# Kernel optimization log

Hardware: AMD Instinct MI355X
Metric: run time of the kernel (lower is better)

Reference implementation:

```python
import jax, jax.numpy as jnp
import numpy as np

D_MODEL = 1024
NUM_HEADS = 16
LN_EPS = 1e-5


def setup_inputs() -> dict:
    key = jax.random.key(0)
    ks = jax.random.split(key, 7)
    B, S, D = 8, 1024, D_MODEL
    x = jax.random.normal(ks[0], (B, S, D), dtype=jnp.float32)
    # LayerNorm params (torch defaults: weight=1, bias=0; randomize slightly)
    ln_gamma = jnp.ones((D,), jnp.float32) + 0.02 * jax.random.normal(ks[1], (D,), jnp.float32)
    ln_beta = 0.02 * jax.random.normal(ks[2], (D,), jnp.float32)
    # nn.MultiheadAttention params: packed in_proj [3D, D], out_proj [D, D]
    scale = 1.0 / np.sqrt(D)
    in_proj_w = scale * jax.random.normal(ks[3], (3 * D, D), dtype=jnp.float32)
    in_proj_b = jnp.zeros((3 * D,), jnp.float32)
    out_proj_w = scale * jax.random.normal(ks[4], (D, D), dtype=jnp.float32)
    out_proj_b = jnp.zeros((D,), jnp.float32)
    return {
        "x": x,
        "ln_gamma": ln_gamma,
        "ln_beta": ln_beta,
        "in_proj_w": in_proj_w,
        "in_proj_b": in_proj_b,
        "out_proj_w": out_proj_w,
        "out_proj_b": out_proj_b,
    }


def reference(x, ln_gamma, ln_beta, in_proj_w, in_proj_b, out_proj_w, out_proj_b):
    B, S, D = x.shape
    H = NUM_HEADS
    Dh = D // H

    residual = x
    # LayerNorm (torch eps=1e-5)
    mu = jnp.mean(x, axis=-1, keepdims=True)
    var = jnp.mean(jnp.square(x - mu), axis=-1, keepdims=True)
    xn = (x - mu) * jax.lax.rsqrt(var + LN_EPS) * ln_gamma + ln_beta

    # Packed QKV projection: y = xn @ in_proj_w.T + in_proj_b
    qkv = jnp.einsum("bsd,ed->bse", xn, in_proj_w) + in_proj_b  # [B,S,3D]
    q, k, v = jnp.split(qkv, 3, axis=-1)

    def heads(t):  # [B,S,D] -> [B,H,S,Dh]
        return t.reshape(B, S, H, Dh).transpose(0, 2, 1, 3)

    q, k, v = heads(q), heads(k), heads(v)

    scores = jnp.einsum("bhsd,bhtd->bhst", q, k) / np.sqrt(Dh)  # [B,H,S,S]
    probs = jax.nn.softmax(scores, axis=-1)
    ctx = jnp.einsum("bhst,bhtd->bhsd", probs, v)  # [B,H,S,Dh]
    ctx = ctx.transpose(0, 2, 1, 3).reshape(B, S, D)

    attn_out = jnp.einsum("bsd,ed->bse", ctx, out_proj_w) + out_proj_b
    # (need_weights=True would also expose probs.mean over heads; math above
    #  matches the explicit non-flash path torch falls back to)
    return attn_out + residual
```

## Files before the change

kernel.cpp:

```cpp
#include <hip/hip_runtime.h>
#include <hip/hip_bf16.h>

typedef __bf16 bf16;
typedef __bf16 bf16x8 __attribute__((ext_vector_type(8)));
typedef __bf16 bf16x4 __attribute__((ext_vector_type(4)));
typedef float  f32x4  __attribute__((ext_vector_type(4)));

#define D_MODEL 1024
#define S_LEN   1024
#define NHEAD   16
#define DH      64

#define AS1 __attribute__((address_space(1)))
#define AS3 __attribute__((address_space(3)))

__global__ __launch_bounds__(256) void ln_cvt_kernel(
        const float* __restrict__ x, const float* __restrict__ gamma,
        const float* __restrict__ beta, bf16* __restrict__ xn,
        const float* __restrict__ w1, bf16* __restrict__ o1, int n1,
        const float* __restrict__ w2, bf16* __restrict__ o2, int n2) {
    const int tid = threadIdx.x;
    if (blockIdx.x < 8192) {
        const int row = blockIdx.x;
        const float4 v = ((const float4*)(x + (size_t)row * D_MODEL))[tid];
        float s  = v.x + v.y + v.z + v.w;
        float s2 = v.x*v.x + v.y*v.y + v.z*v.z + v.w*v.w;
        #pragma unroll
        for (int d = 1; d < 64; d <<= 1) { s += __shfl_xor(s, d); s2 += __shfl_xor(s2, d); }
        __shared__ float red[8];
        const int wave = tid >> 6;
        if ((tid & 63) == 0) { red[wave] = s; red[4 + wave] = s2; }
        __syncthreads();
        s  = red[0] + red[1] + red[2] + red[3];
        s2 = red[4] + red[5] + red[6] + red[7];
        const float mu   = s * (1.0f / D_MODEL);
        const float var  = s2 * (1.0f / D_MODEL) - mu * mu;
        const float rstd = rsqrtf(var + 1e-5f);
        const float4 g = ((const float4*)gamma)[tid];
        const float4 b = ((const float4*)beta)[tid];
        bf16x4 o;
        o[0] = (bf16)((v.x - mu) * rstd * g.x + b.x);
        o[1] = (bf16)((v.y - mu) * rstd * g.y + b.y);
        o[2] = (bf16)((v.z - mu) * rstd * g.z + b.z);
        o[3] = (bf16)((v.w - mu) * rstd * g.w + b.w);
        ((bf16x4*)(xn + (size_t)row * D_MODEL))[tid] = o;
    } else {
        int i = (blockIdx.x - 8192) * 256 + tid;
        const int stride = 1024 * 256;
        for (; i < n1 + n2; i += stride) {
            const float4 v = (i < n1) ? ((const float4*)w1)[i] : ((const float4*)w2)[i - n1];
            bf16x4 r;
            r[0] = (bf16)v.x; r[1] = (bf16)v.y; r[2] = (bf16)v.z; r[3] = (bf16)v.w;
            if (i < n1) ((bf16x4*)o1)[i] = r; else ((bf16x4*)o2)[i - n1] = r;
        }
    }
}

#define GEMM_MAIN_LOOP(Ab, Wb, K)                                                        \
    f32x4 acc[4][4] = {};                                                                \
    for (int kt = 0; kt < (K); kt += 64) {                                               \
        _Pragma("unroll")                                                                \
        for (int i = 0; i < 4; ++i) {                                                    \
            const int L = i * 256 + tid;                                                 \
            const int r = L >> 3, blk = L & 7;                                           \
            const int src = (blk ^ (r & 7)) * 8;                                         \
            __builtin_amdgcn_global_load_lds(                                            \
                (const AS1 void*)((Ab) + (size_t)r * (K) + kt + src),                    \
                (AS3 void*)(As + L * 8), 16, 0, 0);                                      \
            __builtin_amdgcn_global_load_lds(                                            \
                (const AS1 void*)((Wb) + (size_t)r * (K) + kt + src),                    \
                (AS3 void*)(Bs + L * 8), 16, 0, 0);                                      \
        }                                                                                \
        __syncthreads();                                                                 \
        _Pragma("unroll")                                                                \
        for (int kk = 0; kk < 2; ++kk) {                                                 \
            bf16x8 af[4], bfm[4];                                                        \
            _Pragma("unroll")                                                            \
            for (int m = 0; m < 4; ++m) {                                                \
                const int R = wr * 64 + m * 16 + (lane & 15);                            \
                af[m] = *(const bf16x8*)(As + R * 64 +                                   \
                            (((kk * 4 + (lane >> 4)) ^ (R & 7)) << 3));                  \
            }                                                                            \
            _Pragma("unroll")                                                            \
            for (int n = 0; n < 4; ++n) {                                                \
                const int R = wc * 64 + n * 16 + (lane & 15);                            \
                bfm[n] = *(const bf16x8*)(Bs + R * 64 +                                  \
                            (((kk * 4 + (lane >> 4)) ^ (R & 7)) << 3));                  \
            }                                                                            \
            _Pragma("unroll")                                                            \
            for (int m = 0; m < 4; ++m)                                                  \
                _Pragma("unroll")                                                        \
                for (int n = 0; n < 4; ++n)                                              \
                    acc[m][n] = __builtin_amdgcn_mfma_f32_16x16x32_bf16(                 \
                        af[m], bfm[n], acc[m][n], 0, 0, 0);                              \
        }                                                                                \
        __syncthreads();                                                                 \
    }

#define XCD_REMAP()                                                                      \
    const int f = blockIdx.y * gridDim.x + blockIdx.x;                                   \
    const int xcd = f & 7;                                                               \
    const int rank = f >> 3;                                                             \
    const int brow = (xcd * 8 + (rank & 7)) * 128;                                       \
    const int bcol = (rank >> 3) * 128;

__global__ __launch_bounds__(256, 4) void gemm_qkv(
        const bf16* __restrict__ A, const bf16* __restrict__ W,
        const float* __restrict__ bias,
        bf16* __restrict__ q, bf16* __restrict__ k, bf16* __restrict__ vt) {
    __shared__ bf16 smem[2 * 128 * 64];
    bf16* As = smem;
    bf16* Bs = smem + 128 * 64;
    const int tid = threadIdx.x;
    const int lane = tid & 63;
    const int wave = tid >> 6;
    const int wr = wave >> 1, wc = wave & 1;
    XCD_REMAP()
    const bf16* Ab = A + (size_t)brow * 1024;
    const bf16* Wb = W + (size_t)bcol * 1024;

    GEMM_MAIN_LOOP(Ab, Wb, 1024)

    const int region = bcol >> 10;
    const int c = lane & 15, hh = lane >> 4;
    if (region == 2) {
        #pragma unroll
        for (int m = 0; m < 4; ++m) {
            #pragma unroll
            for (int n = 0; n < 4; ++n) {
                const int col = bcol + wc * 64 + n * 16 + c;
                const float bb = bias[col];
                const int e = col & 1023;
                const int h = e >> 6, dh = e & 63;
                const int row0 = brow + wr * 64 + m * 16 + hh * 4;
                const int b = row0 >> 10, s0 = row0 & 1023;
                const int bh = b * NHEAD + h;
                bf16x4 pk;
                #pragma unroll
                for (int j = 0; j < 4; ++j) pk[j] = (bf16)(acc[m][n][j] + bb);
                *(bf16x4*)(vt + ((size_t)bh * DH + dh) * S_LEN + s0) = pk;
            }
        }
    } else {
        const float qsc = (region == 0) ? 0.1803368801111244f : 1.0f;
        #pragma unroll
        for (int m = 0; m < 4; ++m) {
            #pragma unroll
            for (int n = 0; n < 4; ++n) {
                const int col = wc * 64 + n * 16 + c;
                const float bb = bias[bcol + col];
                #pragma unroll
                for (int j = 0; j < 4; ++j) {
                    const int row = wr * 64 + m * 16 + hh * 4 + j;
                    const int pb = (col >> 3) ^ (row & 7);
                    smem[row * 128 + pb * 8 + (col & 7)] = (bf16)((acc[m][n][j] + bb) * qsc);
                }
            }
        }
        __syncthreads();
        bf16* dst = (region == 0) ? q : k;
        #pragma unroll
        for (int i = 0; i < 8; ++i) {
            const int idx = i * 256 + tid;
            const int row = idx >> 4;
            const int bb = idx & 15;
            const bf16x8 vv = *(const bf16x8*)(smem + row * 128 + (bb ^ (row & 7)) * 8);
            const int grow = brow + row;
            const int s = grow & 1023, b = grow >> 10;
            const int col0 = bcol + bb * 8;
            const int e = col0 & 1023;
            const int h = e >> 6, dh = e & 63;
            *(bf16x8*)(dst + ((size_t)(b * NHEAD + h) * S_LEN + s) * DH + dh) = vv;
        }
    }
}

__global__ __launch_bounds__(256, 4) void gemm_out(
        const bf16* __restrict__ A, const bf16* __restrict__ W,
        const float* __restrict__ bias, const float* __restrict__ resid,
        float* __restrict__ out) {
    __shared__ bf16 smem[2 * 128 * 64];
    bf16* As = smem;
    bf16* Bs = smem + 128 * 64;
    const int tid = threadIdx.x;
    const int lane = tid & 63;
    const int wave = tid >> 6;
    const int wr = wave >> 1, wc = wave & 1;
    XCD_REMAP()
    const bf16* Ab = A + (size_t)brow * 1024;
    const bf16* Wb = W + (size_t)bcol * 1024;

    GEMM_MAIN_LOOP(Ab, Wb, 1024)

    #pragma unroll
    for (int m = 0; m < 4; ++m) {
        #pragma unroll
        for (int n = 0; n < 4; ++n) {
            const int col = bcol + wc * 64 + n * 16 + (lane & 15);
            const float bb = bias[col];
            #pragma unroll
            for (int j = 0; j < 4; ++j) {
                const int row = brow + wr * 64 + m * 16 + (lane >> 4) * 4 + j;
                const size_t idx = (size_t)row * D_MODEL + col;
                out[idx] = acc[m][n][j] + bb + resid[idx];
            }
        }
    }
}

__global__ __launch_bounds__(512, 4) void attn_kernel(
        const bf16* __restrict__ Q, const bf16* __restrict__ Kv,
        const bf16* __restrict__ Vt, bf16* __restrict__ ctx) {
    __shared__ bf16 KsB[2][64 * 64];
    __shared__ bf16 VsB[2][64 * 64];
    __shared__ bf16 PtB[8][32 * 64];
    const int tid = threadIdx.x;
    const int lane = tid & 63;
    const int w = tid >> 6;
    const int c = lane & 15;
    const int h = lane >> 4;
    const int bh = blockIdx.x;
    const int bb = bh >> 4, hd = bh & 15;
    const int q0 = blockIdx.y * 256 + w * 32;

    const bf16* Qh = Q + ((size_t)bh * S_LEN + q0) * DH;
    const char* Kb = (const char*)(Kv + (size_t)bh * S_LEN * DH);
    const char* Vb = (const char*)(Vt + (size_t)bh * DH * S_LEN);
    char* pw = (char*)&PtB[w][0];

    bf16x8 qf[2][2];
    #pragma unroll
    for (int nq = 0; nq < 2; ++nq)
        #pragma unroll
        for (int kk = 0; kk < 2; ++kk)
            qf[nq][kk] = *(const bf16x8*)(Qh + (16 * nq + c) * DH + kk * 32 + h * 8);

    bf16x8 ones;
    #pragma unroll
    for (int j = 0; j < 8; ++j) ones[j] = (bf16)1.0f;

    f32x4 O[2][4] = {};
    f32x4 lacc[2] = {};

#define STAGE(BB, KT) do {                                                               \
    const int row = tid >> 3;                                                            \
    const int sw = ((tid & 7) ^ (row & 7)) << 4;                                         \
    __builtin_amdgcn_global_load_lds(                                                    \
        (const AS1 void*)(Kb + (size_t)((KT) + row) * 128 + sw),                         \
        (AS3 void*)((char*)&KsB[BB][0] + tid * 16), 16, 0, 0);                           \
    __builtin_amdgcn_global_load_lds(                                                    \
        (const AS1 void*)(Vb + (size_t)row * 2048 + (KT) * 2 + sw),                      \
        (AS3 void*)((char*)&VsB[BB][0] + tid * 16), 16, 0, 0);                           \
} while (0)

    STAGE(0, 0);
    for (int t = 0; t < 16; ++t) {
        if (t < 15) {
            STAGE((t + 1) & 1, (t + 1) * 64);
            asm volatile("s_waitcnt vmcnt(2)" ::: "memory");
        } else {
            asm volatile("s_waitcnt vmcnt(0)" ::: "memory");
        }
        __builtin_amdgcn_s_barrier();
        const char* Ksb = (const char*)&KsB[t & 1][0];
        const char* Vsb = (const char*)&VsB[t & 1][0];

        f32x4 sf[2][4] = {};
        __builtin_amdgcn_s_setprio(1);
        #pragma unroll
        for (int kk = 0; kk < 2; ++kk) {
            bf16x8 kf[4];
            #pragma unroll
            for (int a = 0; a < 4; ++a)
                kf[a] = *(const bf16x8*)(Ksb + (16 * a + c) * 128 +
                                         (((4 * kk + h) ^ (c & 7)) << 4));
            #pragma unroll
            for (int nq = 0; nq < 2; ++nq)
                #pragma unroll
                for (int a = 0; a < 4; ++a)
                    sf[nq][a] = __builtin_amdgcn_mfma_f32_16x16x32_bf16(
                        kf[a], qf[nq][kk], sf[nq][a], 0, 0, 0);
        }
        __builtin_amdgcn_s_setprio(0);

        #pragma unroll
        for (int nq = 0; nq < 2; ++nq) {
            #pragma unroll
            for (int a = 0; a < 4; ++a) {
                bf16x4 pk;
                #pragma unroll
                for (int r = 0; r < 4; ++r)
                    pk[r] = (bf16)__builtin_amdgcn_exp2f(sf[nq][a][r]);
                *(bf16x4*)(pw + (16 * nq + c) * 128 +
                           (((2 * a + (h >> 1)) ^ (c & 7)) << 4) + 8 * (h & 1)) = pk;
            }
        }

        __builtin_amdgcn_s_setprio(1);
        #pragma unroll
        for (int kk = 0; kk < 2; ++kk) {
            bf16x8 pf[2], vf[4];
            #pragma unroll
            for (int mq = 0; mq < 2; ++mq)
                pf[mq] = *(const bf16x8*)(pw + (16 * mq + c) * 128 +
                                          (((4 * kk + h) ^ (c & 7)) << 4));
            #pragma unroll
            for (int f2 = 0; f2 < 4; ++f2)
                vf[f2] = *(const bf16x8*)(Vsb + (16 * f2 + c) * 128 +
                                          (((4 * kk + h) ^ (c & 7)) << 4));
            #pragma unroll
            for (int mq = 0; mq < 2; ++mq) {
                #pragma unroll
                for (int f2 = 0; f2 < 4; ++f2)
                    O[mq][f2] = __builtin_amdgcn_mfma_f32_16x16x32_bf16(
                        pf[mq], vf[f2], O[mq][f2], 0, 0, 0);
                lacc[mq] = __builtin_amdgcn_mfma_f32_16x16x32_bf16(
                    pf[mq], ones, lacc[mq], 0, 0, 0);
            }
        }
        __builtin_amdgcn_s_setprio(0);
        asm volatile("s_waitcnt lgkmcnt(0)" ::: "memory");
        __builtin_amdgcn_s_barrier();
    }
#undef STAGE

    #pragma unroll
    for (int mq = 0; mq < 2; ++mq) {
        float iv[4];
        #pragma unroll
        for (int r = 0; r < 4; ++r) iv[r] = 1.0f / lacc[mq][r];
        #pragma unroll
        for (int f2 = 0; f2 < 4; ++f2)
            #pragma unroll
            for (int r = 0; r < 4; ++r) {
                const int s = q0 + 16 * mq + 4 * h + r;
                ctx[((size_t)(bb * S_LEN + s)) * D_MODEL + hd * DH + 16 * f2 + c] =
                    (bf16)(O[mq][f2][r] * iv[r]);
            }
    }
}

extern "C" void kernel_launch(void* const* d_in, const int* in_sizes, int n_in,
                              void* d_out, int out_size, void* d_ws, size_t ws_size,
                              hipStream_t stream) {
    const float* x     = (const float*)d_in[0];
    const float* gamma = (const float*)d_in[1];
    const float* beta  = (const float*)d_in[2];
    const float* in_w  = (const float*)d_in[3];
    const float* in_b  = (const float*)d_in[4];
    const float* out_w = (const float*)d_in[5];
    const float* out_b = (const float*)d_in[6];
    float* out = (float*)d_out;

    char* ws = (char*)d_ws;
    bf16* wq  = (bf16*)(ws);
    bf16* wo  = (bf16*)(ws + 6291456);
    bf16* xn  = (bf16*)(ws + 8388608);
    bf16* q   = (bf16*)(ws + 25165824);
    bf16* kk  = (bf16*)(ws + 41943040);
    bf16* vt  = (bf16*)(ws + 58720256);
    bf16* ctx = xn;

    hipLaunchKernelGGL(ln_cvt_kernel, dim3(9216), dim3(256), 0, stream,
                       x, gamma, beta, xn,
                       in_w, wq, 3072 * 1024 / 4, out_w, wo, 1024 * 1024 / 4);
    hipLaunchKernelGGL(gemm_qkv, dim3(64, 24), dim3(256), 0, stream, xn, wq, in_b, q, kk, vt);
    hipLaunchKernelGGL(attn_kernel, dim3(128, 4), dim3(512), 0, stream, q, kk, vt, ctx);
    hipLaunchKernelGGL(gemm_out, dim3(64, 8), dim3(256), 0, stream, ctx, wo, out_b, x, out);
}
```

Measured before the change: 140.9 us.

## Stage out-proj epilogue through LDS and halve attention P buffer

The output GEMM epilogue now writes accumulators plus bias into a swizzled LDS tile, one half at a time, then reads back rows to do coalesced float4 residual loads and output stores. This replaces scattered scalar global accesses. Separately, the attention kernel processes the P tile in two 32-column halves, interleaving exp/store with PV MFMAs. That halves the per-wave P shared buffer, and launch bounds rise to 6 blocks per CU to use the freed LDS for occupancy. Risks are extra barriers in the epilogue and register pressure from the higher occupancy target.

```diff
diff --git a/kernel.cpp b/kernel.cpp
--- a/kernel.cpp
+++ b/kernel.cpp
@@ -192,28 +192,49 @@
 
     GEMM_MAIN_LOOP(Ab, Wb, 1024)
 
+    float* fs = (float*)smem;
+    const int c = lane & 15, hh = lane >> 4;
     #pragma unroll
-    for (int m = 0; m < 4; ++m) {
-        #pragma unroll
-        for (int n = 0; n < 4; ++n) {
-            const int col = bcol + wc * 64 + n * 16 + (lane & 15);
-            const float bb = bias[col];
-            #pragma unroll
-            for (int j = 0; j < 4; ++j) {
-                const int row = brow + wr * 64 + m * 16 + (lane >> 4) * 4 + j;
-                const size_t idx = (size_t)row * D_MODEL + col;
-                out[idx] = acc[m][n][j] + bb + resid[idx];
-            }
-        }
-    }
-}
-
-__global__ __launch_bounds__(512, 4) void attn_kernel(
+    for (int half = 0; half < 2; ++half) {
+        if (wr == half) {
+            #pragma unroll
+            for (int m = 0; m < 4; ++m)
+                #pragma unroll
+                for (int n = 0; n < 4; ++n) {
+                    const int col = wc * 64 + n * 16 + c;
+                    const float bb = bias[bcol + col];
+                    #pragma unroll
+                    for (int j = 0; j < 4; ++j) {
+                        const int row = m * 16 + hh * 4 + j;
+                        const int blk = (col >> 2) ^ (row & 7);
+                        fs[row * 128 + blk * 4 + (col & 3)] = acc[m][n][j] + bb;
+                    }
+                }
+        }
+        __syncthreads();
+        #pragma unroll
+        for (int i = 0; i < 8; ++i) {
+            const int idx = i * 256 + tid;
+            const int row = idx >> 5;
+            const int blk = idx & 31;
+            const f32x4 v = *(const f32x4*)(fs + row * 128 + ((blk ^ (row & 7)) << 2));
+            const int grow = brow + half * 64 + row;
+            const int gcol = bcol + blk * 4;
+            const float4 rs = *(const float4*)(resid + (size_t)grow * D_MODEL + gcol);
+            float4 o;
+            o.x = v[0] + rs.x; o.y = v[1] + rs.y; o.z = v[2] + rs.z; o.w = v[3] + rs.w;
+            *(float4*)(out + (size_t)grow * D_MODEL + gcol) = o;
+        }
+        __syncthreads();
+    }
+}
+
+__global__ __launch_bounds__(512, 6) void attn_kernel(
         const bf16* __restrict__ Q, const bf16* __restrict__ Kv,
         const bf16* __restrict__ Vt, bf16* __restrict__ ctx) {
     __shared__ bf16 KsB[2][64 * 64];
     __shared__ bf16 VsB[2][64 * 64];
-    __shared__ bf16 PtB[8][32 * 64];
+    __shared__ bf16 PtB[8][32 * 32];
     const int tid = threadIdx.x;
     const int lane = tid & 63;
     const int w = tid >> 6;
@@ -284,30 +305,30 @@
         __builtin_amdgcn_s_setprio(0);
 
         #pragma unroll
-        for (int nq = 0; nq < 2; ++nq) {
-            #pragma unroll
-            for (int a = 0; a < 4; ++a) {
-                bf16x4 pk;
-                #pragma unroll
-                for (int r = 0; r < 4; ++r)
-                    pk[r] = (bf16)__builtin_amdgcn_exp2f(sf[nq][a][r]);
-                *(bf16x4*)(pw + (16 * nq + c) * 128 +
-                           (((2 * a + (h >> 1)) ^ (c & 7)) << 4) + 8 * (h & 1)) = pk;
-            }
-        }
-
-        __builtin_amdgcn_s_setprio(1);
-        #pragma unroll
-        for (int kk = 0; kk < 2; ++kk) {
+        for (int hf = 0; hf < 2; ++hf) {
+            #pragma unroll
+            for (int nq = 0; nq < 2; ++nq) {
+                #pragma unroll
+                for (int aa = 0; aa < 2; ++aa) {
+                    const int a = hf * 2 + aa;
+                    bf16x4 pk;
+                    #pragma unroll
+                    for (int r = 0; r < 4; ++r)
+                        pk[r] = (bf16)__builtin_amdgcn_exp2f(sf[nq][a][r]);
+                    *(bf16x4*)(pw + (16 * nq + c) * 64 +
+                               (((2 * aa + (h >> 1)) ^ (c & 3)) << 4) + 8 * (h & 1)) = pk;
+                }
+            }
             bf16x8 pf[2], vf[4];
             #pragma unroll
             for (int mq = 0; mq < 2; ++mq)
-                pf[mq] = *(const bf16x8*)(pw + (16 * mq + c) * 128 +
-                                          (((4 * kk + h) ^ (c & 7)) << 4));
+                pf[mq] = *(const bf16x8*)(pw + (16 * mq + c) * 64 +
+                                          ((h ^ (c & 3)) << 4));
             #pragma unroll
             for (int f2 = 0; f2 < 4; ++f2)
                 vf[f2] = *(const bf16x8*)(Vsb + (16 * f2 + c) * 128 +
-                                          (((4 * kk + h) ^ (c & 7)) << 4));
+                                          (((4 * hf + h) ^ (c & 7)) << 4));
+            __builtin_amdgcn_s_setprio(1);
             #pragma unroll
             for (int mq = 0; mq < 2; ++mq) {
                 #pragma unroll
@@ -317,8 +338,8 @@
                 lacc[mq] = __builtin_amdgcn_mfma_f32_16x16x32_bf16(
                     pf[mq], ones, lacc[mq], 0, 0, 0);
             }
-        }
-        __builtin_amdgcn_s_setprio(0);
+            __builtin_amdgcn_s_setprio(0);
+        }
         asm volatile("s_waitcnt lgkmcnt(0)" ::: "memory");
         __builtin_amdgcn_s_barrier();
     }
```

New measurement: 373.1 us. 2.65x slower.
